# Kernel optimization log

Hardware: AMD Instinct MI355X
Metric: run time of the kernel (lower is better)

Reference implementation:

```python
import jax, jax.numpy as jnp
import numpy as np
from jax import lax

NUM_CNNS = 300
INPUT_LEN = 608
NUM_CLASSES = 50
FILTER = 19
POOL = 7
HIDDEN = 100
BATCH = 256
L_CONV = INPUT_LEN - FILTER + 1          # 590
L_POOL = (L_CONV - POOL) // POOL + 1     # 84
EPS = 1e-5


def setup_inputs() -> dict:
    key = jax.random.key(0)
    ks = jax.random.split(key, 24)
    U, H = NUM_CNNS, HIDDEN
    d = {}
    d["x"] = jax.random.normal(ks[0], (BATCH, 4, INPUT_LEN), dtype=jnp.float32)
    # conv1: grouped Conv1d(4*U -> U, k=19, groups=U) on replicated input == dense Conv1d(4 -> U)
    d["w1"] = jax.random.normal(ks[1], (U, 4, FILTER), dtype=jnp.float32) * 0.1
    d["b1"] = jax.random.normal(ks[2], (U,), dtype=jnp.float32) * 0.05
    d["g1"] = jax.random.uniform(ks[3], (U,), dtype=jnp.float32, minval=0.5, maxval=1.5)
    d["be1"] = jax.random.normal(ks[4], (U,), dtype=jnp.float32) * 0.05
    d["m1"] = jax.random.normal(ks[5], (U,), dtype=jnp.float32) * 0.05
    d["v1"] = jax.random.uniform(ks[6], (U,), dtype=jnp.float32, minval=0.5, maxval=1.5)
    # grouped 1x1 conv: per-unit Linear 84 -> 100
    d["w2"] = jax.random.normal(ks[7], (U, H, L_POOL), dtype=jnp.float32) * (1.0 / np.sqrt(L_POOL))
    d["b2"] = jax.random.normal(ks[8], (U, H), dtype=jnp.float32) * 0.05
    d["g2"] = jax.random.uniform(ks[9], (U, H), dtype=jnp.float32, minval=0.5, maxval=1.5)
    d["be2"] = jax.random.normal(ks[10], (U, H), dtype=jnp.float32) * 0.05
    d["m2"] = jax.random.normal(ks[11], (U, H), dtype=jnp.float32) * 0.05
    d["v2"] = jax.random.uniform(ks[12], (U, H), dtype=jnp.float32, minval=0.5, maxval=1.5)
    # grouped 1x1 conv: per-unit Linear 100 -> 1
    d["w3"] = jax.random.normal(ks[13], (U, H), dtype=jnp.float32) * (1.0 / np.sqrt(H))
    d["b3"] = jax.random.normal(ks[14], (U,), dtype=jnp.float32) * 0.05
    d["g3"] = jax.random.uniform(ks[15], (U,), dtype=jnp.float32, minval=0.5, maxval=1.5)
    d["be3"] = jax.random.normal(ks[16], (U,), dtype=jnp.float32) * 0.05
    d["m3"] = jax.random.normal(ks[17], (U,), dtype=jnp.float32) * 0.05
    d["v3"] = jax.random.uniform(ks[18], (U,), dtype=jnp.float32, minval=0.5, maxval=1.5)
    # final Linear(U -> num_classes)
    d["wf"] = jax.random.normal(ks[19], (NUM_CLASSES, U), dtype=jnp.float32) * (1.0 / np.sqrt(U))
    d["bf"] = jax.random.normal(ks[20], (NUM_CLASSES,), dtype=jnp.float32) * 0.05
    return d


def _bn(y, g, be, m, v):
    return (y - m) * (g * lax.rsqrt(v + EPS)) + be


def reference(x, w1, b1, g1, be1, m1, v1, w2, b2, g2, be2, m2, v2,
              w3, b3, g3, be3, m3, v3, wf, bf):
    # conv1 (replicate + grouped conv == dense conv over 4 channels)
    y = lax.conv_general_dilated(x, w1, window_strides=(1,), padding='VALID',
                                 dimension_numbers=('NCH', 'OIH', 'NCH'))  # [B,U,590]
    y = y + b1[None, :, None]
    y = _bn(y, g1[None, :, None], be1[None, :, None], m1[None, :, None], v1[None, :, None])
    y = jnp.exp(y)  # ExpActivation
    # MaxPool1d(7,7): 590 -> 84 (uses first 588 positions)
    B = y.shape[0]
    y = y[:, :, :L_POOL * POOL].reshape(B, NUM_CNNS, L_POOL, POOL).max(axis=-1)  # [B,U,84]
    # per-unit MLP 84 -> 100 (grouped 1x1 conv) + BN + ReLU (dropout is eval-mode identity)
    h = jnp.einsum('buf,uof->buo', y, w2) + b2[None]  # [B,U,100]
    h = _bn(h, g2[None], be2[None], m2[None], v2[None])
    h = jax.nn.relu(h)
    # per-unit 100 -> 1 + BN + ReLU
    z = jnp.einsum('buo,uo->bu', h, w3) + b3[None]  # [B,U]
    z = _bn(z, g3[None], be3[None], m3[None], v3[None])
    z = jax.nn.relu(z)
    # final Linear
    return z @ wf.T + bf
```

## Files before the change

kernel.cpp:

```cpp
#include <hip/hip_runtime.h>
#include <hip/hip_bf16.h>

#define BATCH    256
#define NU       300
#define LIN      608
#define FILT     19
#define LPOOL    84
#define POOL     7
#define HID      100
#define NCLS     50
#define EPS      1e-5f
#define KP       96
#define NP       112
#define LDK      104
#define WROW     104
#define WBROWS   320
#define TCHUNK   112
#define CROW     116
#define MTN      19
#define BH       128

typedef __attribute__((ext_vector_type(8))) short short8;
typedef __attribute__((ext_vector_type(4))) float float4v;

__device__ __forceinline__ unsigned short f2bf(float f) {
    unsigned u = __float_as_uint(f);
    u += 0x7fffu + ((u >> 16) & 1u);
    return (unsigned short)(u >> 16);
}
__device__ __forceinline__ float bf2f(unsigned short h) {
    return __uint_as_float(((unsigned)h) << 16);
}

__global__ void k_prep(const float* __restrict__ w1, const float* __restrict__ x,
                       unsigned short* __restrict__ Wbh,
                       unsigned short* __restrict__ Wbl,
                       unsigned int* __restrict__ xc)
{
    const int idx = blockIdx.x * 256 + threadIdx.x;
    const int NW = WBROWS * WROW;
    if (idx < NW) {
        const int u = idx / WROW, kk = idx - u * WROW;
        float wv = 0.f;
        if (u < NU && kk < 96) {
            const int c = kk / 24, tap = kk - 24 * c;
            if (tap < FILT) wv = w1[(u * 4 + c) * FILT + tap];
        }
        const unsigned short hi = f2bf(wv);
        Wbh[idx] = hi;
        Wbl[idx] = f2bf(wv - bf2f(hi));
    }
    const int j = idx - NW;
    if (j >= 0 && j < BATCH * 4 * LIN) {
        const float xv = x[j];
        const unsigned short hi = f2bf(xv);
        const unsigned short lo = f2bf(xv - bf2f(hi));
        xc[j] = (unsigned)hi | ((unsigned)lo << 16);
    }
}

__global__ __launch_bounds__(256, 2)
void k_conv5(const unsigned short* __restrict__ Wbh,
             const unsigned short* __restrict__ Wbl,
             const unsigned int* __restrict__ xc,
             const float* __restrict__ b1, const float* __restrict__ g1,
             const float* __restrict__ be1, const float* __restrict__ m1,
             const float* __restrict__ v1,
             unsigned short* __restrict__ ypool)
{
    __shared__ __align__(16) unsigned short Bh[TCHUNK * LDK];
    __shared__ __align__(16) unsigned short Bl[TCHUNK * LDK];
    __shared__ float Cs[4][8 * CROW];
    __shared__ float s1s[MTN * 16], c1s[MTN * 16];

    const int tid = threadIdx.x;
    const int b   = blockIdx.x;
    const int tc  = blockIdx.y;
    const int t0  = TCHUNK * tc;
    const int NT  = (tc == 5) ? 2 : 7;

    for (int i = tid; i < TCHUNK * 12; i += 256) {
        const int trow = i / 12;
        if (trow >= 16 * NT) continue;
        const int rem   = i - 12 * trow;
        const int c     = rem / 3;
        const int third = rem - 3 * c;
        const int kkb   = 24 * c + 8 * third;
        const int tt0   = t0 + trow + 8 * third;
        const unsigned int* src = xc + ((b * 4 + c) * LIN + tt0);

        unsigned int w[8];
        if (third < 2 && tt0 + 8 <= LIN) {
            const uint4 v0 = *(const uint4*)(src);
            const uint4 v1 = *(const uint4*)(src + 4);
            w[0] = v0.x; w[1] = v0.y; w[2] = v0.z; w[3] = v0.w;
            w[4] = v1.x; w[5] = v1.y; w[6] = v1.z; w[7] = v1.w;
        } else {
#pragma unroll
            for (int j = 0; j < 8; ++j) {
                const int tap = 8 * third + j;
                const int tt  = tt0 + j;
                unsigned int v = 0;
                if (tap < FILT && tt < LIN) v = src[j];
                w[j] = v;
            }
        }
        short8 hv, lv;
#pragma unroll
        for (int j = 0; j < 8; ++j) {
            hv[j] = (short)(w[j] & 0xffffu);
            lv[j] = (short)(w[j] >> 16);
        }
        *(short8*)(&Bh[trow * LDK + kkb]) = hv;
        *(short8*)(&Bl[trow * LDK + kkb]) = lv;
    }
    for (int i = tid; i < MTN * 16; i += 256) {
        if (i < NU) {
            const float s = g1[i] * rsqrtf(v1[i] + EPS);
            s1s[i] = s;
            c1s[i] = (b1[i] - m1[i]) * s + be1[i];
        } else { s1s[i] = 0.f; c1s[i] = 0.f; }
    }
    __syncthreads();

    const int lane = tid & 63;
    const int n    = lane & 15;
    const int quad = lane >> 4;
    const int wave = tid >> 6;
    float* Csw = Cs[wave];

    for (int mt = wave; mt < MTN; mt += 4) {
        const unsigned short* wrh = Wbh + (size_t)(mt * 16 + n) * WROW;
        const unsigned short* wrl = Wbl + (size_t)(mt * 16 + n) * WROW;
        short8 afh[3], afl[3];
#pragma unroll
        for (int s = 0; s < 3; ++s) {
            afh[s] = *(const short8*)(wrh + 32 * s + 8 * quad);
            afl[s] = *(const short8*)(wrl + 32 * s + 8 * quad);
        }

        float4v acc[7];
#pragma unroll
        for (int nt = 0; nt < 7; ++nt) {
            acc[nt] = (float4v){0.f, 0.f, 0.f, 0.f};
            if (nt < NT) {
                short8 bhf[3], blf[3];
#pragma unroll
                for (int s = 0; s < 3; ++s) {
                    bhf[s] = *(const short8*)(&Bh[(16 * nt + n) * LDK + 32 * s + 8 * quad]);
                    blf[s] = *(const short8*)(&Bl[(16 * nt + n) * LDK + 32 * s + 8 * quad]);
                }
#pragma unroll
                for (int s = 0; s < 3; ++s)
                    acc[nt] = __builtin_amdgcn_mfma_f32_16x16x32_bf16(
                        afh[s], bhf[s], acc[nt], 0, 0, 0);
#pragma unroll
                for (int s = 0; s < 3; ++s)
                    acc[nt] = __builtin_amdgcn_mfma_f32_16x16x32_bf16(
                        afh[s], blf[s], acc[nt], 0, 0, 0);
#pragma unroll
                for (int s = 0; s < 3; ++s)
                    acc[nt] = __builtin_amdgcn_mfma_f32_16x16x32_bf16(
                        afl[s], bhf[s], acc[nt], 0, 0, 0);
            }
        }

#pragma unroll
        for (int half = 0; half < 2; ++half) {
            __builtin_amdgcn_fence(__ATOMIC_ACQ_REL, "workgroup");
            if ((quad >> 1) == half) {
                const int lrow = (quad & 1) * 4;
#pragma unroll
                for (int nt = 0; nt < 7; ++nt) {
                    if (nt < NT) {
#pragma unroll
                        for (int r = 0; r < 4; ++r)
                            Csw[(lrow + r) * CROW + 16 * nt + n] = acc[nt][r];
                    }
                }
            }
            __builtin_amdgcn_fence(__ATOMIC_ACQ_REL, "workgroup");
#pragma unroll
            for (int rep = 0; rep < 2; ++rep) {
                const int id = rep * 64 + lane;
                const int ul = id & 7;
                const int p  = id >> 3;
                const int uglob = mt * 16 + half * 8 + ul;
                if (uglob < NU) {
                    const int pg = 16 * tc + p;
                    unsigned short outv = 0;
                    if (pg < LPOOL) {
                        const float* row = &Csw[ul * CROW + 7 * p];
                        float mx = row[0];
#pragma unroll
                        for (int j = 1; j < 7; ++j) mx = fmaxf(mx, row[j]);
                        outv = f2bf(__expf(fmaf(mx, s1s[uglob], c1s[uglob])));
                    }
                    if (pg < KP)
                        ypool[((size_t)uglob * BATCH + b) * KP + pg] = outv;
                }
            }
        }
    }
}

__global__ __launch_bounds__(256, 3)
void k_mlp(const unsigned short* __restrict__ ypool,
           const float* __restrict__ w2, const float* __restrict__ b2,
           const float* __restrict__ g2, const float* __restrict__ be2,
           const float* __restrict__ m2, const float* __restrict__ v2,
           const float* __restrict__ w3, const float* __restrict__ b3,
           const float* __restrict__ g3, const float* __restrict__ be3,
           const float* __restrict__ m3, const float* __restrict__ v3,
           float* __restrict__ zbuf)
{
    __shared__ __align__(16) unsigned short As[NP * LDK];
    __shared__ __align__(16) unsigned short Bs[BH * LDK];
    __shared__ __align__(16) float4 cs4[NP];

    const int tid = threadIdx.x;
    const int u   = blockIdx.x;
    const int b0  = blockIdx.y * BH;

    {
        const float* src = w2 + (size_t)u * HID * LPOOL;
        for (int c = tid; c < HID * (LPOOL / 4); c += 256) {
            const int o  = c / (LPOOL / 4);
            const int kc = (c % (LPOOL / 4)) * 4;
            const float4 v = *(const float4*)(src + o * LPOOL + kc);
            unsigned short* d = &As[o * LDK + kc];
            d[0] = f2bf(v.x); d[1] = f2bf(v.y); d[2] = f2bf(v.z); d[3] = f2bf(v.w);
        }
        for (int c = tid; c < HID * 6; c += 256) {
            const int o = c / 6, kc = LPOOL + (c % 6) * 2;
            *(unsigned*)(&As[o * LDK + kc]) = 0;
        }
        for (int c = tid; c < (NP - HID) * (KP / 2); c += 256) {
            const int o = HID + c / (KP / 2), kc = (c % (KP / 2)) * 2;
            *(unsigned*)(&As[o * LDK + kc]) = 0;
        }
    }
    {
        const unsigned short* ys = ypool + ((size_t)u * BATCH + b0) * KP;
        for (int c = tid; c < BH * (KP / 8); c += 256) {
            const int n  = c / (KP / 8);
            const int kc = (c % (KP / 8)) * 8;
            *(short8*)(&Bs[n * LDK + kc]) = *(const short8*)(ys + n * KP + kc);
        }
    }
    if (tid < NP) {
        float4 cv = {0.f, 0.f, 0.f, 0.f};
        if (tid < HID) {
            const int uo = u * HID + tid;
            const float s = g2[uo] * rsqrtf(v2[uo] + EPS);
            cv.x = s;
            cv.y = (b2[uo] - m2[uo]) * s + be2[uo];
            cv.z = w3[uo];
        }
        cs4[tid] = cv;
    }
    __syncthreads();

    const int lane = tid & 63;
    const int wave = tid >> 6;
    const int col  = lane & 15;
    const int quad = lane >> 4;

    short8 bf_[2][3];
#pragma unroll
    for (int j = 0; j < 2; ++j) {
        const int brow = 16 * (2 * wave + j) + col;
#pragma unroll
        for (int s = 0; s < 3; ++s)
            bf_[j][s] = *(const short8*)(&Bs[brow * LDK + 32 * s + 8 * quad]);
    }

    float zp0 = 0.f, zp1 = 0.f;
#pragma unroll
    for (int mt = 0; mt < 7; ++mt) {
        short8 af[3];
#pragma unroll
        for (int s = 0; s < 3; ++s)
            af[s] = *(const short8*)(&As[(16 * mt + col) * LDK + 32 * s + 8 * quad]);

        float4v a0 = {0.f, 0.f, 0.f, 0.f}, a1 = {0.f, 0.f, 0.f, 0.f};
#pragma unroll
        for (int s = 0; s < 3; ++s) {
            a0 = __builtin_amdgcn_mfma_f32_16x16x32_bf16(af[s], bf_[0][s], a0, 0, 0, 0);
            a1 = __builtin_amdgcn_mfma_f32_16x16x32_bf16(af[s], bf_[1][s], a1, 0, 0, 0);
        }
#pragma unroll
        for (int r = 0; r < 4; ++r) {
            const float4 cv = cs4[16 * mt + 4 * quad + r];
            zp0 = fmaf(fmaxf(fmaf(a0[r], cv.x, cv.y), 0.f), cv.z, zp0);
            zp1 = fmaf(fmaxf(fmaf(a1[r], cv.x, cv.y), 0.f), cv.z, zp1);
        }
    }

    zp0 += __shfl_xor(zp0, 16); zp0 += __shfl_xor(zp0, 32);
    zp1 += __shfl_xor(zp1, 16); zp1 += __shfl_xor(zp1, 32);

    if (quad == 0) {
        const float s3 = g3[u] * rsqrtf(v3[u] + EPS);
        const float c3 = (b3[u] - m3[u]) * s3 + be3[u];
        const int bA = b0 + 16 * (2 * wave + 0) + col;
        const int bB = b0 + 16 * (2 * wave + 1) + col;
        zbuf[(size_t)u * BATCH + bA] = fmaxf(fmaf(zp0, s3, c3), 0.f);
        zbuf[(size_t)u * BATCH + bB] = fmaxf(fmaf(zp1, s3, c3), 0.f);
    }
}

__global__ __launch_bounds__(256, 4)
void k_final(const float* __restrict__ zbuf, const float* __restrict__ wf,
             const float* __restrict__ bf, float* __restrict__ out)
{
    __shared__ float red[4][64];
    const int nc   = blockIdx.x;
    const int bq   = blockIdx.y;
    const int lane = threadIdx.x & 63;
    const int wave = threadIdx.x >> 6;
    const int b    = bq * 64 + lane;

    float a0 = 0.f, a1 = 0.f, a2 = 0.f;
    const int u0 = wave * 75;
#pragma unroll 5
    for (int i = 0; i < 75; i += 3) {
        a0 = fmaf(zbuf[(size_t)(u0 + i + 0) * BATCH + b], wf[nc * NU + u0 + i + 0], a0);
        a1 = fmaf(zbuf[(size_t)(u0 + i + 1) * BATCH + b], wf[nc * NU + u0 + i + 1], a1);
        a2 = fmaf(zbuf[(size_t)(u0 + i + 2) * BATCH + b], wf[nc * NU + u0 + i + 2], a2);
    }
    red[wave][lane] = (a0 + a1) + a2;
    __syncthreads();
    if (threadIdx.x < 64) {
        const float s = (red[0][lane] + red[1][lane]) + (red[2][lane] + red[3][lane]);
        out[(size_t)b * NCLS + nc] = s + bf[nc];
    }
}

extern "C" void kernel_launch(void* const* d_in, const int* in_sizes, int n_in,
                              void* d_out, int out_size, void* d_ws, size_t ws_size,
                              hipStream_t stream)
{
    const float* x   = (const float*)d_in[0];
    const float* w1  = (const float*)d_in[1];
    const float* b1  = (const float*)d_in[2];
    const float* g1  = (const float*)d_in[3];
    const float* be1 = (const float*)d_in[4];
    const float* m1  = (const float*)d_in[5];
    const float* v1  = (const float*)d_in[6];
    const float* w2  = (const float*)d_in[7];
    const float* b2  = (const float*)d_in[8];
    const float* g2  = (const float*)d_in[9];
    const float* be2 = (const float*)d_in[10];
    const float* m2  = (const float*)d_in[11];
    const float* v2  = (const float*)d_in[12];
    const float* w3  = (const float*)d_in[13];
    const float* b3  = (const float*)d_in[14];
    const float* g3  = (const float*)d_in[15];
    const float* be3 = (const float*)d_in[16];
    const float* m3  = (const float*)d_in[17];
    const float* v3  = (const float*)d_in[18];
    const float* wf  = (const float*)d_in[19];
    const float* bf  = (const float*)d_in[20];

    unsigned short* ypool = (unsigned short*)d_ws;
    float* zbuf = (float*)((char*)d_ws + 14745600);
    unsigned short* Wbh = (unsigned short*)((char*)d_ws + 15052800);
    unsigned short* Wbl = (unsigned short*)((char*)d_ws + 15119360);
    unsigned int*   xc  = (unsigned int*)((char*)d_ws + 15185920);

    const int prep_elems = WBROWS * WROW + BATCH * 4 * LIN;
    k_prep<<<(prep_elems + 255) / 256, 256, 0, stream>>>(w1, x, Wbh, Wbl, xc);

    dim3 gc(BATCH, 6);
    k_conv5<<<gc, 256, 0, stream>>>(Wbh, Wbl, xc, b1, g1, be1, m1, v1, ypool);

    dim3 gm(NU, BATCH / BH);
    k_mlp<<<gm, 256, 0, stream>>>(ypool, w2, b2, g2, be2, m2, v2,
                                  w3, b3, g3, be3, m3, v3, zbuf);

    dim3 gf(NCLS, 4);
    k_final<<<gf, 256, 0, stream>>>(zbuf, wf, bf, (float*)d_out);
}
```

Baseline: 166.3 us.

## Process two M-tiles per wave in conv kernel, reuse B fragments, shrink LDS

Each wave in the conv kernel now computes two 16-unit output tiles per iteration, so every B fragment loaded from LDS feeds twice as many MFMAs. The per-block BN scale/shift precompute is moved into the prep kernel and read from global memory as float2. The epilogue staging buffer is relaid out as float4 stores per column, with four passes over quads. Together with the smaller LDS footprint this allows 3 blocks per CU instead of 2. The cost is more accumulator registers (14 float4 per wave) and four fence-separated epilogue passes instead of two.

```diff
diff --git a/kernel.cpp b/kernel.cpp
--- a/kernel.cpp
+++ b/kernel.cpp
@@ -16,7 +16,6 @@
 #define WROW     104
 #define WBROWS   320
 #define TCHUNK   112
-#define CROW     116
 #define MTN      19
 #define BH       128
 
@@ -33,9 +32,13 @@
 }
 
 __global__ void k_prep(const float* __restrict__ w1, const float* __restrict__ x,
+                       const float* __restrict__ b1, const float* __restrict__ g1,
+                       const float* __restrict__ be1, const float* __restrict__ m1,
+                       const float* __restrict__ v1,
                        unsigned short* __restrict__ Wbh,
                        unsigned short* __restrict__ Wbl,
-                       unsigned int* __restrict__ xc)
+                       unsigned int* __restrict__ xc,
+                       float2* __restrict__ s1c1)
 {
     const int idx = blockIdx.x * 256 + threadIdx.x;
     const int NW = WBROWS * WROW;
@@ -57,21 +60,28 @@
         const unsigned short lo = f2bf(xv - bf2f(hi));
         xc[j] = (unsigned)hi | ((unsigned)lo << 16);
     }
-}
-
-__global__ __launch_bounds__(256, 2)
-void k_conv5(const unsigned short* __restrict__ Wbh,
+    const int j2 = j - BATCH * 4 * LIN;
+    if (j2 >= 0 && j2 < MTN * 16) {
+        float2 v = {0.f, 0.f};
+        if (j2 < NU) {
+            const float s = g1[j2] * rsqrtf(v1[j2] + EPS);
+            v.x = s;
+            v.y = (b1[j2] - m1[j2]) * s + be1[j2];
+        }
+        s1c1[j2] = v;
+    }
+}
+
+__global__ __launch_bounds__(256, 3)
+void k_conv6(const unsigned short* __restrict__ Wbh,
              const unsigned short* __restrict__ Wbl,
              const unsigned int* __restrict__ xc,
-             const float* __restrict__ b1, const float* __restrict__ g1,
-             const float* __restrict__ be1, const float* __restrict__ m1,
-             const float* __restrict__ v1,
+             const float2* __restrict__ s1c1,
              unsigned short* __restrict__ ypool)
 {
     __shared__ __align__(16) unsigned short Bh[TCHUNK * LDK];
     __shared__ __align__(16) unsigned short Bl[TCHUNK * LDK];
-    __shared__ float Cs[4][8 * CROW];
-    __shared__ float s1s[MTN * 16], c1s[MTN * 16];
+    __shared__ __align__(16) float Cs[4][TCHUNK * 4];
 
     const int tid = threadIdx.x;
     const int b   = blockIdx.x;
@@ -114,13 +124,6 @@
         *(short8*)(&Bh[trow * LDK + kkb]) = hv;
         *(short8*)(&Bl[trow * LDK + kkb]) = lv;
     }
-    for (int i = tid; i < MTN * 16; i += 256) {
-        if (i < NU) {
-            const float s = g1[i] * rsqrtf(v1[i] + EPS);
-            s1s[i] = s;
-            c1s[i] = (b1[i] - m1[i]) * s + be1[i];
-        } else { s1s[i] = 0.f; c1s[i] = 0.f; }
-    }
     __syncthreads();
 
     const int lane = tid & 63;
@@ -129,20 +132,41 @@
     const int wave = tid >> 6;
     float* Csw = Cs[wave];
 
-    for (int mt = wave; mt < MTN; mt += 4) {
-        const unsigned short* wrh = Wbh + (size_t)(mt * 16 + n) * WROW;
-        const unsigned short* wrl = Wbl + (size_t)(mt * 16 + n) * WROW;
-        short8 afh[3], afl[3];
-#pragma unroll
-        for (int s = 0; s < 3; ++s) {
-            afh[s] = *(const short8*)(wrh + 32 * s + 8 * quad);
-            afl[s] = *(const short8*)(wrl + 32 * s + 8 * quad);
-        }
-
-        float4v acc[7];
+    const int ep_ul = lane & 3;
+    const int ep_p  = lane >> 2;
+
+    for (int k = wave; k < 10; k += 4) {
+        const int mt0 = 2 * k;
+        const bool two = (mt0 + 1 < MTN);
+
+        short8 a0h[3], a0l[3], a1h[3], a1l[3];
+        {
+            const unsigned short* wrh = Wbh + (size_t)(mt0 * 16 + n) * WROW;
+            const unsigned short* wrl = Wbl + (size_t)(mt0 * 16 + n) * WROW;
+#pragma unroll
+            for (int s = 0; s < 3; ++s) {
+                a0h[s] = *(const short8*)(wrh + 32 * s + 8 * quad);
+                a0l[s] = *(const short8*)(wrl + 32 * s + 8 * quad);
+            }
+            const int m1r = two ? (mt0 + 1) : mt0;
+            const unsigned short* wrh1 = Wbh + (size_t)(m1r * 16 + n) * WROW;
+            const unsigned short* wrl1 = Wbl + (size_t)(m1r * 16 + n) * WROW;
+#pragma unroll
+            for (int s = 0; s < 3; ++s) {
+                a1h[s] = *(const short8*)(wrh1 + 32 * s + 8 * quad);
+                a1l[s] = *(const short8*)(wrl1 + 32 * s + 8 * quad);
+            }
+        }
+
+        float4v acc[2][7];
+#pragma unroll
+        for (int t2 = 0; t2 < 2; ++t2)
+#pragma unroll
+            for (int nt = 0; nt < 7; ++nt)
+                acc[t2][nt] = (float4v){0.f, 0.f, 0.f, 0.f};
+
 #pragma unroll
         for (int nt = 0; nt < 7; ++nt) {
-            acc[nt] = (float4v){0.f, 0.f, 0.f, 0.f};
             if (nt < NT) {
                 short8 bhf[3], blf[3];
 #pragma unroll
@@ -152,49 +176,60 @@
                 }
 #pragma unroll
                 for (int s = 0; s < 3; ++s)
-                    acc[nt] = __builtin_amdgcn_mfma_f32_16x16x32_bf16(
-                        afh[s], bhf[s], acc[nt], 0, 0, 0);
+                    acc[0][nt] = __builtin_amdgcn_mfma_f32_16x16x32_bf16(
+                        a0h[s], bhf[s], acc[0][nt], 0, 0, 0);
 #pragma unroll
                 for (int s = 0; s < 3; ++s)
-                    acc[nt] = __builtin_amdgcn_mfma_f32_16x16x32_bf16(
-                        afh[s], blf[s], acc[nt], 0, 0, 0);
+                    acc[0][nt] = __builtin_amdgcn_mfma_f32_16x16x32_bf16(
+                        a0h[s], blf[s], acc[0][nt], 0, 0, 0);
 #pragma unroll
                 for (int s = 0; s < 3; ++s)
-                    acc[nt] = __builtin_amdgcn_mfma_f32_16x16x32_bf16(
-                        afl[s], bhf[s], acc[nt], 0, 0, 0);
+                    acc[0][nt] = __builtin_amdgcn_mfma_f32_16x16x32_bf16(
+                        a0l[s], bhf[s], acc[0][nt], 0, 0, 0);
+                if (two) {
+#pragma unroll
+                    for (int s = 0; s < 3; ++s)
+                        acc[1][nt] = __builtin_amdgcn_mfma_f32_16x16x32_bf16(
+                            a1h[s], bhf[s], acc[1][nt], 0, 0, 0);
+#pragma unroll
+                    for (int s = 0; s < 3; ++s)
+                        acc[1][nt] = __builtin_amdgcn_mfma_f32_16x16x32_bf16(
+                            a1h[s], blf[s], acc[1][nt], 0, 0, 0);
+#pragma unroll
+                    for (int s = 0; s < 3; ++s)
+                        acc[1][nt] = __builtin_amdgcn_mfma_f32_16x16x32_bf16(
+                            a1l[s], bhf[s], acc[1][nt], 0, 0, 0);
+                }
             }
         }
 
 #pragma unroll
-        for (int half = 0; half < 2; ++half) {
-            __builtin_amdgcn_fence(__ATOMIC_ACQ_REL, "workgroup");
-            if ((quad >> 1) == half) {
-                const int lrow = (quad & 1) * 4;
-#pragma unroll
-                for (int nt = 0; nt < 7; ++nt) {
-                    if (nt < NT) {
-#pragma unroll
-                        for (int r = 0; r < 4; ++r)
-                            Csw[(lrow + r) * CROW + 16 * nt + n] = acc[nt][r];
+        for (int t2 = 0; t2 < 2; ++t2) {
+            if (t2 == 1 && !two) break;
+            const int mt = mt0 + t2;
+#pragma unroll
+            for (int qq = 0; qq < 4; ++qq) {
+                __builtin_amdgcn_fence(__ATOMIC_ACQ_REL, "workgroup");
+                if (quad == qq) {
+#pragma unroll
+                    for (int nt = 0; nt < 7; ++nt) {
+                        if (nt < NT)
+                            *(float4v*)(&Csw[(16 * nt + n) * 4]) = acc[t2][nt];
                     }
                 }
-            }
-            __builtin_amdgcn_fence(__ATOMIC_ACQ_REL, "workgroup");
-#pragma unroll
-            for (int rep = 0; rep < 2; ++rep) {
-                const int id = rep * 64 + lane;
-                const int ul = id & 7;
-                const int p  = id >> 3;
-                const int uglob = mt * 16 + half * 8 + ul;
+                __builtin_amdgcn_fence(__ATOMIC_ACQ_REL, "workgroup");
+
+                const int uglob = mt * 16 + 4 * qq + ep_ul;
+                const int pg    = 16 * tc + ep_p;
                 if (uglob < NU) {
-                    const int pg = 16 * tc + p;
                     unsigned short outv = 0;
                     if (pg < LPOOL) {
-                        const float* row = &Csw[ul * CROW + 7 * p];
-                        float mx = row[0];
-#pragma unroll
-                        for (int j = 1; j < 7; ++j) mx = fmaxf(mx, row[j]);
-                        outv = f2bf(__expf(fmaf(mx, s1s[uglob], c1s[uglob])));
+                        float mx = Csw[(7 * ep_p) * 4 + ep_ul];
+#pragma unroll
+                        for (int j = 1; j < 7; ++j)
+                            mx = fmaxf(mx, Csw[(7 * ep_p + j) * 4 + ep_ul]);
+                        const float2 sc = s1c1[uglob];
+                        outv = f2bf(__expf(fmaf(mx, sc.x, sc.y)));
                     }
                     if (pg < KP)
                         ypool[((size_t)uglob * BATCH + b) * KP + pg] = outv;
@@ -368,12 +403,14 @@
     unsigned short* Wbh = (unsigned short*)((char*)d_ws + 15052800);
     unsigned short* Wbl = (unsigned short*)((char*)d_ws + 15119360);
     unsigned int*   xc  = (unsigned int*)((char*)d_ws + 15185920);
-
-    const int prep_elems = WBROWS * WROW + BATCH * 4 * LIN;
-    k_prep<<<(prep_elems + 255) / 256, 256, 0, stream>>>(w1, x, Wbh, Wbl, xc);
+    float2*         sc1 = (float2*)((char*)d_ws + 17676288);
+
+    const int prep_elems = WBROWS * WROW + BATCH * 4 * LIN + MTN * 16;
+    k_prep<<<(prep_elems + 255) / 256, 256, 0, stream>>>(
+        w1, x, b1, g1, be1, m1, v1, Wbh, Wbl, xc, sc1);
 
     dim3 gc(BATCH, 6);
-    k_conv5<<<gc, 256, 0, stream>>>(Wbh, Wbl, xc, b1, g1, be1, m1, v1, ypool);
+    k_conv6<<<gc, 256, 0, stream>>>(Wbh, Wbl, xc, sc1, ypool);
 
     dim3 gm(NU, BATCH / BH);
     k_mlp<<<gm, 256, 0, stream>>>(ypool, w2, b2, g2, be2, m2, v2,
```

Measured after the change: 161.3 us. 3.0% less time.
